# Optimization experiments

Measured on AMD Instinct MI355X. Metric: run time of the kernel, lower is better.

The kernel has to match this reference:

```python
import math
import jax, jax.numpy as jnp
import numpy as np

B, T, C = 4, 2048, 1024
H = 16
HS = C // H  # head_size = 64

def setup_inputs() -> dict:
    key = jax.random.key(0)
    k1, k2, k3 = jax.random.split(key, 3)
    x = jax.random.normal(k1, (B, T, C), dtype=jnp.float32)
    W_qkv = jax.random.normal(k2, (C, 3 * C), dtype=jnp.float32) * (1.0 / math.sqrt(C))
    W_proj = jax.random.normal(k3, (C, C), dtype=jnp.float32) * (1.0 / math.sqrt(C))
    b_proj = jnp.zeros((C,), dtype=jnp.float32)
    return {"x": x, "W_qkv": W_qkv, "W_proj": W_proj, "b_proj": b_proj}

def reference(x, W_qkv, W_proj, b_proj):
    Bx, Tx, Cx = x.shape
    qkv = x @ W_qkv  # [B,T,3C]
    q, k, v = jnp.split(qkv, 3, axis=-1)
    # [B,T,C] -> [B,H,T,HS]
    def heads(t):
        return t.reshape(Bx, Tx, H, HS).transpose(0, 2, 1, 3)
    q, k, v = heads(q), heads(k), heads(v)
    scores = jnp.einsum('bhqd,bhkd->bhqk', q, k) / math.sqrt(HS)
    causal = jnp.tril(jnp.ones((Tx, Tx), dtype=bool))
    scores = jnp.where(causal, scores, -jnp.inf)
    attn = jax.nn.softmax(scores, axis=-1)
    out = jnp.einsum('bhqk,bhkd->bhqd', attn, v)  # [B,H,T,HS]
    out = out.transpose(0, 2, 1, 3).reshape(Bx, Tx, Cx)
    return out @ W_proj + b_proj
```

## Files before the change

### kernel.cpp

```cpp
#include <hip/hip_runtime.h>
#include <hip/hip_bf16.h>
#include <cstdint>
#include <cstddef>

using bf16 = __hip_bfloat16;
typedef __attribute__((ext_vector_type(8))) short short8;
typedef __attribute__((ext_vector_type(4))) float floatx4;

#define B_ 4
#define T_ 2048
#define C_ 1024
#define H_ 16
#define HS_ 64
#define BT_ (B_*T_)
#define N3C (3*C_)

#define MFMA16(a,b,c) __builtin_amdgcn_mfma_f32_16x16x32_bf16((a),(b),(c),0,0,0)

#if __has_builtin(__builtin_amdgcn_exp2f)
#define EXP2(x) __builtin_amdgcn_exp2f(x)
#else
#define EXP2(x) exp2f(x)
#endif

static __device__ __forceinline__ void gld16(const bf16* g, bf16* l) {
  __builtin_amdgcn_global_load_lds(
      (const __attribute__((address_space(1))) unsigned int*)g,
      (__attribute__((address_space(3))) unsigned int*)l, 16, 0, 0);
}

static __device__ __forceinline__ unsigned short f2bf_us(float x) {
  bf16 b = __float2bfloat16(x);
  return *(unsigned short*)&b;
}

__global__ __launch_bounds__(256)
void k_prep(const float* __restrict__ x, bf16* __restrict__ xb,
            const float* __restrict__ Wqkv, bf16* __restrict__ wqkvT,
            const float* __restrict__ Wproj, bf16* __restrict__ wprojT)
{
  const int bid = blockIdx.x, tid = threadIdx.x;
  __shared__ float tile[64][65];

  if (bid < 4096) {
    const int i = bid*256 + tid;
    const float4 v0 = ((const float4*)x)[2*i];
    const float4 v1 = ((const float4*)x)[2*i + 1];
    union { bf16 b[8]; uint4 u; } cvt;
    cvt.b[0] = __float2bfloat16(v0.x);
    cvt.b[1] = __float2bfloat16(v0.y);
    cvt.b[2] = __float2bfloat16(v0.z);
    cvt.b[3] = __float2bfloat16(v0.w);
    cvt.b[4] = __float2bfloat16(v1.x);
    cvt.b[5] = __float2bfloat16(v1.y);
    cvt.b[6] = __float2bfloat16(v1.z);
    cvt.b[7] = __float2bfloat16(v1.w);
    ((uint4*)xb)[i] = cvt.u;
    return;
  }

  const float* in; bf16* out; int N, n0, k0;
  if (bid < 4864) {
    const int j = bid - 4096;
    in = Wqkv; out = wqkvT; N = N3C;
    n0 = (j % 48) * 64; k0 = (j / 48) * 64;
  } else {
    const int j = bid - 4864;
    in = Wproj; out = wprojT; N = C_;
    n0 = (j % 16) * 64; k0 = (j / 16) * 64;
  }
  const int r = tid >> 6, c = tid & 63;
  #pragma unroll
  for (int j = 0; j < 16; ++j)
    tile[r + j*4][c] = in[(size_t)(k0 + r + j*4) * N + n0 + c];
  __syncthreads();
  #pragma unroll
  for (int j = 0; j < 16; ++j) {
    int rr = r + j*4;
    out[(size_t)(n0 + rr) * C_ + k0 + c] = __float2bfloat16(tile[c][rr]);
  }
}

__global__ __launch_bounds__(512, 1)
void k_gemm256(const bf16* __restrict__ A, const bf16* __restrict__ Bt,
               bf16* __restrict__ Qb, bf16* __restrict__ Kb, bf16* __restrict__ Vt)
{
  __shared__ __align__(16) char smem[65536];
  bf16* const sA = (bf16*)smem;
  bf16* const sB = (bf16*)(smem + 32768);

  const int tid  = threadIdx.x;
  const int lane = tid & 63, wave = tid >> 6;
  const int quad = lane >> 4, l16 = lane & 15;
  const int wm = wave >> 2, wn = wave & 3;

  const int g = blockIdx.x;
  const int xcd = g & 7;
  const int local = g >> 3;
  const int nb = local % 12;
  const int mb = (local / 12) * 8 + xcd;
  const int m0 = mb * 256, n0 = nb * 256;

  const int ra = tid >> 2;
  const int gc = (tid & 3) ^ (ra & 3);
  const bf16* aptr = A  + (size_t)(m0 + ra) * C_ + gc*8;
  const bf16* bptr = Bt + (size_t)(n0 + ra) * C_ + gc*8;

  floatx4 acc[8][4] = {};
  const int aoff = (wm*128 + l16)*32 + (quad ^ (l16 & 3))*8;
  const int boff = (wn*64  + l16)*32 + (quad ^ (l16 & 3))*8;

  gld16(aptr,            sA + tid*8);
  gld16(aptr + 128*C_,   sA + 4096 + tid*8);
  gld16(bptr,            sB + tid*8);
  gld16(bptr + 128*C_,   sB + 4096 + tid*8);

  for (int i = 0; i < 32; ++i) {
    const int cur = i & 1;
    if (i + 1 < 32) {
      const int k0 = (i + 1) * 32;
      bf16* sa = sA + (cur ^ 1) * 8192;
      bf16* sb = sB + (cur ^ 1) * 8192;
      gld16(aptr + k0,           sa + tid*8);
      gld16(aptr + 128*C_ + k0,  sa + 4096 + tid*8);
      gld16(bptr + k0,           sb + tid*8);
      gld16(bptr + 128*C_ + k0,  sb + 4096 + tid*8);
      asm volatile("s_waitcnt vmcnt(4)" ::: "memory");
    } else {
      asm volatile("s_waitcnt vmcnt(0)" ::: "memory");
    }
    asm volatile("s_barrier" ::: "memory");
    const bf16* sa = sA + cur * 8192;
    const bf16* sb = sB + cur * 8192;
    short8 a0[4], bq[4], a1[4];
    #pragma unroll
    for (int ii = 0; ii < 4; ++ii) a0[ii] = *(const short8*)&sa[aoff + ii*512];
    #pragma unroll
    for (int j = 0; j < 4; ++j)   bq[j]  = *(const short8*)&sb[boff + j*512];
    __builtin_amdgcn_s_setprio(1);
    #pragma unroll
    for (int ii = 0; ii < 4; ++ii)
      #pragma unroll
      for (int j = 0; j < 4; ++j)
        acc[ii][j] = MFMA16(a0[ii], bq[j], acc[ii][j]);
    __builtin_amdgcn_s_setprio(0);
    #pragma unroll
    for (int ii = 0; ii < 4; ++ii) a1[ii] = *(const short8*)&sa[aoff + 2048 + ii*512];
    asm volatile("s_barrier" ::: "memory");
    __builtin_amdgcn_s_setprio(1);
    #pragma unroll
    for (int ii = 0; ii < 4; ++ii)
      #pragma unroll
      for (int j = 0; j < 4; ++j)
        acc[4+ii][j] = MFMA16(a1[ii], bq[j], acc[4+ii][j]);
    __builtin_amdgcn_s_setprio(0);
    asm volatile("s_barrier" ::: "memory");
  }

  if (nb >= 8) {
    unsigned short* epi = (unsigned short*)smem;
    const int b  = m0 >> 11;
    const int t0 = m0 & 2047;
    #pragma unroll 1
    for (int pass = 0; pass < 4; ++pass) {
      if (wn == pass) {
        #pragma unroll
        for (int ii = 0; ii < 8; ++ii) {
          const int tl = wm*128 + ii*16 + quad*4;
          #pragma unroll
          for (int j = 0; j < 4; ++j) {
            const int ccl = j*16 + l16;
            #pragma unroll
            for (int r = 0; r < 4; ++r)
              epi[ccl*264 + tl + r] = f2bf_us(acc[ii][j][r]);
          }
        }
      }
      __syncthreads();
      const int h = ((n0 - 2*C_) >> 6) + pass;
      #pragma unroll
      for (int it = 0; it < 16; ++it) {
        const int id = it*512 + tid;
        const int tp = id & 31;
        const int rest = id >> 5;
        const int tl64 = (rest & 3) * 64;
        const int ccl = rest >> 2;
        const int k0p = tp + (tp & 16);
        const unsigned lo = epi[ccl*264 + tl64 + k0p];
        const unsigned hi = epi[ccl*264 + tl64 + k0p + 16];
        unsigned* row = (unsigned*)(Vt + ((size_t)(b*H_ + h) * HS_ + ccl) * T_);
        row[(t0 >> 1) + tl64/2 + tp] = lo | (hi << 16);
      }
      if (pass < 3) __syncthreads();
    }
  } else {
    #pragma unroll
    for (int ii = 0; ii < 8; ++ii) {
      const int rowb = m0 + wm*128 + ii*16 + quad*4;
      #pragma unroll
      for (int j = 0; j < 4; ++j) {
        const int col = n0 + wn*64 + j*16 + l16;
        const int h = (col >> 6) & 15, d = col & 63;
        #pragma unroll
        for (int r = 0; r < 4; ++r) {
          const float v = acc[ii][j][r];
          const int rr = rowb + r;
          const int bb = rr >> 11, t = rr & 2047;
          const size_t addr = (((size_t)(bb*H_ + h) * T_ + t) << 6) + d;
          if (nb < 4) {
            Qb[addr] = __float2bfloat16(v * 0.18033688f);
          } else {
            Kb[addr] = __float2bfloat16(v);
          }
        }
      }
    }
  }
}

template<int MODE, int NB>
__global__ __launch_bounds__(256, 2)
void k_gemm(const bf16* __restrict__ A, const bf16* __restrict__ Bt,
            int N, int K,
            bf16* __restrict__ Qb, bf16* __restrict__ Kb, bf16* __restrict__ Vt,
            float* __restrict__ Out, const float* __restrict__ bias)
{
  __shared__ __align__(16) char smem[65536];
  bf16* const sAb = (bf16*)smem;
  bf16* const sBb = (bf16*)(smem + 32768);

  const int tid  = threadIdx.x;
  const int lane = tid & 63, wave = tid >> 6;
  const int quad = lane >> 4, l16 = lane & 15;
  const int wm = wave >> 1, wn = wave & 1;

  const int g = blockIdx.x;
  const int xcd = g & 7;
  const int local = g >> 3;
  const int nb = local % NB;
  const int mb = (local / NB) * 8 + xcd;
  const int m0 = mb * 128, n0 = nb * 128;

  const int ra = tid >> 3;
  const int gc = (tid & 7) ^ (ra & 7);
  const bf16* aptr = A  + (size_t)(m0 + ra) * K + gc*8;
  const bf16* bptr = Bt + (size_t)(n0 + ra) * K + gc*8;
  const size_t rj = (size_t)32 * K;

  floatx4 acc[4][4] = {};
  const int KI = K >> 6;
  const int x7a = l16 & 7;

  for (int i = 0; i <= KI; ++i) {
    __syncthreads();
    if (i < KI) {
      const int k0 = i << 6;
      bf16* sa = sAb + (i & 1) * 8192;
      bf16* sb = sBb + (i & 1) * 8192;
      #pragma unroll
      for (int q2 = 0; q2 < 4; ++q2) {
        gld16(aptr + q2*rj + k0, sa + q2*2048 + tid*8);
        gld16(bptr + q2*rj + k0, sb + q2*2048 + tid*8);
      }
    }
    if (i == 0) continue;
    const bf16* sa = sAb + ((i-1) & 1) * 8192;
    const bf16* sb = sBb + ((i-1) & 1) * 8192;
    #pragma unroll
    for (int ks = 0; ks < 2; ++ks) {
      short8 af[4], bfm[4];
      #pragma unroll
      for (int ii = 0; ii < 4; ++ii)
        af[ii] = *(const short8*)&sa[(wm*64 + ii*16 + l16)*64 + ((ks*4 + quad) ^ x7a)*8];
      #pragma unroll
      for (int ii = 0; ii < 4; ++ii)
        bfm[ii] = *(const short8*)&sb[(wn*64 + ii*16 + l16)*64 + ((ks*4 + quad) ^ x7a)*8];
      #pragma unroll
      for (int ii = 0; ii < 4; ++ii)
        #pragma unroll
        for (int j = 0; j < 4; ++j)
          acc[ii][j] = MFMA16(af[ii], bfm[j], acc[ii][j]);
    }
  }

  #pragma unroll
  for (int i = 0; i < 4; ++i) {
    const int rowb = m0 + wm*64 + i*16 + quad*4;
    #pragma unroll
    for (int j = 0; j < 4; ++j) {
      const int col = n0 + wn*64 + j*16 + l16;
      #pragma unroll
      for (int r = 0; r < 4; ++r) {
        const float v = acc[i][j][r];
        const int rr = rowb + r;
        if (MODE == 1) {
          Out[(size_t)rr * N + col] = v + bias[col];
        }
      }
    }
  }
}

__global__ __launch_bounds__(256, 3)
void k_attn(const bf16* __restrict__ Q, const bf16* __restrict__ K,
            const bf16* __restrict__ Vt, bf16* __restrict__ att)
{
  __shared__ bf16 kbuf[2][64*64];
  __shared__ bf16 vbuf[2][64*64];
  __shared__ bf16 pbuf[4][32*64];

  const int tid  = threadIdx.x;
  const int lane = tid & 63, wave = tid >> 6;
  const int quad = lane >> 4, l16 = lane & 15;
  const int x7 = l16 & 7;

  const int g  = blockIdx.x;
  const int bh = (g & 7) * 8 + ((g >> 3) & 7);
  const int qt = 15 - (g >> 6);
  const int b = bh >> 4, h = bh & 15;

  const bf16* Qp = Q  + (size_t)bh * T_ * HS_;
  const bf16* Kp = K  + (size_t)bh * T_ * HS_;
  const bf16* Vp = Vt + (size_t)bh * HS_ * T_;

  const int qbase = qt*128 + wave*32;
  const int ntk = 2*qt + 2;

  short8 qf[2][2];
  #pragma unroll
  for (int mt = 0; mt < 2; ++mt)
    #pragma unroll
    for (int ss = 0; ss < 2; ++ss)
      qf[mt][ss] = *(const short8*)(Qp + (size_t)(qbase + mt*16 + l16) * HS_ + ss*32 + quad*8);

  floatx4 o[2][4] = {};
  float lrow[2][4] = {};

  const bf16* kg[2]; const bf16* vg[2];
  int ldsoff[2];
  #pragma unroll
  for (int it = 0; it < 2; ++it) {
    const int c = it*256 + tid;
    const int row = c >> 3;
    const int col = (c & 7) ^ (row & 7);
    kg[it] = Kp + (size_t)row * HS_ + col*8;
    vg[it] = Vp + (size_t)row * T_ + col*8;
    ldsoff[it] = c*8;
  }

  bf16* pw = pbuf[wave];
  unsigned int* pw32 = (unsigned int*)pw;
  const int c0 = l16 >> 2;
  const int dwl = l16 & 3;

  for (int i = 0; i <= ntk; ++i) {
    __syncthreads();
    if (i < ntk) {
      const int stk0 = i * 64;
      bf16* kb = kbuf[i & 1];
      bf16* vb = vbuf[i & 1];
      #pragma unroll
      for (int it = 0; it < 2; ++it) {
        gld16(kg[it] + (size_t)stk0 * HS_, kb + ldsoff[it]);
        gld16(vg[it] + stk0,               vb + ldsoff[it]);
      }
    }
    if (i == 0) continue;
    const int tk  = i - 1;
    const int tk0 = tk * 64;
    if (tk0 > qbase + 31) continue;
    const bf16* kb = kbuf[tk & 1];
    const bf16* vb = vbuf[tk & 1];

    floatx4 s[2][4] = {};
    __builtin_amdgcn_s_setprio(1);
    #pragma unroll
    for (int nt = 0; nt < 4; ++nt) {
      const int key = nt*16 + l16;
      #pragma unroll
      for (int ss = 0; ss < 2; ++ss) {
        short8 kf = *(const short8*)&kb[(key*8 + ((ss*4+quad) ^ x7))*8];
        s[0][nt] = MFMA16(qf[0][ss], kf, s[0][nt]);
        s[1][nt] = MFMA16(qf[1][ss], kf, s[1][nt]);
      }
    }
    __builtin_amdgcn_s_setprio(0);

    if (tk0 + 63 > qbase) {
      #pragma unroll
      for (int mt = 0; mt < 2; ++mt)
        #pragma unroll
        for (int nt = 0; nt < 4; ++nt) {
          const int key = tk0 + nt*16 + l16;
          #pragma unroll
          for (int r = 0; r < 4; ++r) {
            const int qr = qbase + mt*16 + quad*4 + r;
            if (key > qr) s[mt][nt][r] = -1e30f;
          }
        }
    }

    #pragma unroll
    for (int mt = 0; mt < 2; ++mt) {
      #pragma unroll
      for (int r = 0; r < 4; ++r) {
        const float p0 = EXP2(s[mt][0][r]), p1 = EXP2(s[mt][1][r]);
        const float p2 = EXP2(s[mt][2][r]), p3 = EXP2(s[mt][3][r]);
        lrow[mt][r] += (p0 + p1) + (p2 + p3);
        const int q = mt*16 + quad*4 + r;
        const unsigned w0 = __builtin_amdgcn_perm(__float_as_uint(p1), __float_as_uint(p0), 0x07060302u);
        const unsigned w1 = __builtin_amdgcn_perm(__float_as_uint(p3), __float_as_uint(p2), 0x07060302u);
        pw32[q*32 + (((c0 + q)     & 7) << 2) + dwl] = w0;
        pw32[q*32 + (((c0 + q + 4) & 7) << 2) + dwl] = w1;
      }
    }

    __builtin_amdgcn_s_setprio(1);
    #pragma unroll
    for (int ss = 0; ss < 2; ++ss) {
      short8 pf0 = *(const short8*)&pw[l16*64      + ((4*ss + quad + l16) & 7)*8];
      short8 pf1 = *(const short8*)&pw[(16+l16)*64 + ((4*ss + quad + l16) & 7)*8];
      #pragma unroll
      for (int nd = 0; nd < 4; ++nd) {
        const int d = nd*16 + l16;
        short8 vf = *(const short8*)&vb[(d*8 + ((ss*4+quad) ^ x7))*8];
        o[0][nd] = MFMA16(pf0, vf, o[0][nd]);
        o[1][nd] = MFMA16(pf1, vf, o[1][nd]);
      }
    }
    __builtin_amdgcn_s_setprio(0);
  }

  #pragma unroll
  for (int mt = 0; mt < 2; ++mt) {
    #pragma unroll
    for (int r = 0; r < 4; ++r) {
      float lsum = lrow[mt][r];
      lsum += __shfl_xor(lsum, 1);
      lsum += __shfl_xor(lsum, 2);
      lsum += __shfl_xor(lsum, 4);
      lsum += __shfl_xor(lsum, 8);
      const float inv = 1.0f / lsum;
      const int tt = qbase + mt*16 + quad*4 + r;
      #pragma unroll
      for (int nd = 0; nd < 4; ++nd)
        att[(size_t)(b*T_ + tt) * C_ + h*64 + nd*16 + l16] =
            __float2bfloat16(o[mt][nd][r] * inv);
    }
  }
}

extern "C" void kernel_launch(void* const* d_in, const int* in_sizes, int n_in,
                              void* d_out, int out_size, void* d_ws, size_t ws_size,
                              hipStream_t stream) {
  const float* x     = (const float*)d_in[0];
  const float* Wqkv  = (const float*)d_in[1];
  const float* Wproj = (const float*)d_in[2];
  const float* bproj = (const float*)d_in[3];
  float* out = (float*)d_out;

  char* ws = (char*)d_ws;
  bf16* xb     = (bf16*)(ws + 0);
  bf16* wqkvT  = (bf16*)(ws + 16777216);
  bf16* wprojT = (bf16*)(ws + 23068672);
  bf16* Qb     = (bf16*)(ws + 25165824);
  bf16* Kb     = (bf16*)(ws + 41943040);
  bf16* Vt     = (bf16*)(ws + 58720256);
  bf16* att    = (bf16*)(ws + 75497472);

  k_prep<<<dim3(5120), 256, 0, stream>>>(x, xb, Wqkv, wqkvT, Wproj, wprojT);
  k_gemm256<<<dim3(384), 512, 0, stream>>>(xb, wqkvT, Qb, Kb, Vt);
  k_attn<<<dim3(1024), 256, 0, stream>>>(Qb, Kb, Vt, att);
  k_gemm<1, 8><<<dim3(512), 256, 0, stream>>>(
      att, wprojT, C_, C_, nullptr, nullptr, nullptr, out, bproj);
}
```

Before: 239.9 us.

## Deepen QKV GEMM pipeline to four LDS stages with split A/B prefetch

The QKV projection GEMM moves from double-buffered LDS to a four-stage ring buffer with three K-slices prefetched ahead. Loads for A and B are issued separately, interleaved between the two MFMA halves of each iteration, which drops one barrier per iteration. The LDS swizzle pattern also changes to reduce bank conflicts. LDS use grows to 128KB per block, and a sync is added before the epilogue reuses shared memory.

Measured after the change: 229.1 us. -4.5%, faster.

```diff
diff --git a/kernel.cpp b/kernel.cpp
--- a/kernel.cpp
+++ b/kernel.cpp
@@ -85,9 +85,9 @@
 void k_gemm256(const bf16* __restrict__ A, const bf16* __restrict__ Bt,
                bf16* __restrict__ Qb, bf16* __restrict__ Kb, bf16* __restrict__ Vt)
 {
-  __shared__ __align__(16) char smem[65536];
+  __shared__ __align__(16) char smem[131072];
   bf16* const sA = (bf16*)smem;
-  bf16* const sB = (bf16*)(smem + 32768);
+  bf16* const sB = (bf16*)(smem + 65536);
 
   const int tid  = threadIdx.x;
   const int lane = tid & 63, wave = tid >> 6;
@@ -102,62 +102,64 @@
   const int m0 = mb * 256, n0 = nb * 256;
 
   const int ra = tid >> 2;
-  const int gc = (tid & 3) ^ (ra & 3);
+  const int gc = (tid & 3) ^ ((ra >> 1) & 3);
   const bf16* aptr = A  + (size_t)(m0 + ra) * C_ + gc*8;
   const bf16* bptr = Bt + (size_t)(n0 + ra) * C_ + gc*8;
 
   floatx4 acc[8][4] = {};
-  const int aoff = (wm*128 + l16)*32 + (quad ^ (l16 & 3))*8;
-  const int boff = (wn*64  + l16)*32 + (quad ^ (l16 & 3))*8;
-
-  gld16(aptr,            sA + tid*8);
-  gld16(aptr + 128*C_,   sA + 4096 + tid*8);
-  gld16(bptr,            sB + tid*8);
-  gld16(bptr + 128*C_,   sB + 4096 + tid*8);
-
+  const int swz = (l16 >> 1) & 3;
+  const int aoff = (wm*128 + l16)*32 + (quad ^ swz)*8;
+  const int boff = (wn*64  + l16)*32 + (quad ^ swz)*8;
+
+#define STAGE_A(t) { bf16* d = sA + ((t)&3)*8192;                       \
+    gld16(aptr + (t)*32,            d + tid*8);                         \
+    gld16(aptr + (size_t)128*C_ + (t)*32, d + 4096 + tid*8); }
+#define STAGE_B(t) { bf16* d = sB + ((t)&3)*8192;                       \
+    gld16(bptr + (t)*32,            d + tid*8);                         \
+    gld16(bptr + (size_t)128*C_ + (t)*32, d + 4096 + tid*8); }
+
+  STAGE_A(0); STAGE_B(0);
+  STAGE_A(1); STAGE_B(1);
+  STAGE_A(2); STAGE_B(2);
+
+  #pragma unroll 1
   for (int i = 0; i < 32; ++i) {
-    const int cur = i & 1;
-    if (i + 1 < 32) {
-      const int k0 = (i + 1) * 32;
-      bf16* sa = sA + (cur ^ 1) * 8192;
-      bf16* sb = sB + (cur ^ 1) * 8192;
-      gld16(aptr + k0,           sa + tid*8);
-      gld16(aptr + 128*C_ + k0,  sa + 4096 + tid*8);
-      gld16(bptr + k0,           sb + tid*8);
-      gld16(bptr + 128*C_ + k0,  sb + 4096 + tid*8);
-      asm volatile("s_waitcnt vmcnt(4)" ::: "memory");
-    } else {
-      asm volatile("s_waitcnt vmcnt(0)" ::: "memory");
-    }
+    if (i < 30)       asm volatile("s_waitcnt vmcnt(8)" ::: "memory");
+    else if (i == 30) asm volatile("s_waitcnt vmcnt(4)" ::: "memory");
+    else              asm volatile("s_waitcnt vmcnt(0)" ::: "memory");
     asm volatile("s_barrier" ::: "memory");
-    const bf16* sa = sA + cur * 8192;
-    const bf16* sb = sB + cur * 8192;
-    short8 a0[4], bq[4], a1[4];
-    #pragma unroll
-    for (int ii = 0; ii < 4; ++ii) a0[ii] = *(const short8*)&sa[aoff + ii*512];
-    #pragma unroll
-    for (int j = 0; j < 4; ++j)   bq[j]  = *(const short8*)&sb[boff + j*512];
+    const bf16* sa = sA + (i & 3)*8192;
+    const bf16* sb = sB + (i & 3)*8192;
+    short8 bq[4], af[4];
+    #pragma unroll
+    for (int j = 0; j < 4; ++j)    bq[j]  = *(const short8*)&sb[boff + j*512];
+    #pragma unroll
+    for (int ii = 0; ii < 4; ++ii) af[ii] = *(const short8*)&sa[aoff + ii*512];
+    if (i <= 28) STAGE_A(i+3);
     __builtin_amdgcn_s_setprio(1);
     #pragma unroll
     for (int ii = 0; ii < 4; ++ii)
       #pragma unroll
       for (int j = 0; j < 4; ++j)
-        acc[ii][j] = MFMA16(a0[ii], bq[j], acc[ii][j]);
-    __builtin_amdgcn_s_setprio(0);
-    #pragma unroll
-    for (int ii = 0; ii < 4; ++ii) a1[ii] = *(const short8*)&sa[aoff + 2048 + ii*512];
-    asm volatile("s_barrier" ::: "memory");
-    __builtin_amdgcn_s_setprio(1);
-    #pragma unroll
-    for (int ii = 0; ii < 4; ++ii)
-      #pragma unroll
-      for (int j = 0; j < 4; ++j)
-        acc[4+ii][j] = MFMA16(a1[ii], bq[j], acc[4+ii][j]);
+        acc[ii][j] = MFMA16(af[ii], bq[j], acc[ii][j]);
     __builtin_amdgcn_s_setprio(0);
     asm volatile("s_barrier" ::: "memory");
-  }
+    #pragma unroll
+    for (int ii = 0; ii < 4; ++ii) af[ii] = *(const short8*)&sa[aoff + 2048 + ii*512];
+    if (i <= 28) STAGE_B(i+3);
+    __builtin_amdgcn_s_setprio(1);
+    #pragma unroll
+    for (int ii = 0; ii < 4; ++ii)
+      #pragma unroll
+      for (int j = 0; j < 4; ++j)
+        acc[4+ii][j] = MFMA16(af[ii], bq[j], acc[4+ii][j]);
+    __builtin_amdgcn_s_setprio(0);
+  }
+#undef STAGE_A
+#undef STAGE_B
 
   if (nb >= 8) {
+    __syncthreads();
     unsigned short* epi = (unsigned short*)smem;
     const int b  = m0 >> 11;
     const int t0 = m0 & 2047;
```
